# Kernel tuning notes

Hardware: AMD Instinct MI355X
Metric: run time of the kernel (lower is better)

The kernel has to match this reference:

```python
import jax, jax.numpy as jnp
import numpy as np

K = 20        # kNN neighborhood size (args.k)
EPS = 1e-5    # BatchNorm eps
SLOPE = 0.2   # LeakyReLU negative slope
B, N = 8, 2048


def lrelu(x):
    return jnp.where(x >= 0, x, SLOPE * x)


def bn_cn(x):  # BatchNorm1d over [B, C, N] (training-mode batch stats, gamma=1, beta=0)
    m = jnp.mean(x, axis=(0, 2), keepdims=True)
    v = jnp.var(x, axis=(0, 2), keepdims=True)
    return (x - m) * jax.lax.rsqrt(v + EPS)


def bn_f(x):  # BatchNorm1d over [B, F]
    m = jnp.mean(x, axis=0, keepdims=True)
    v = jnp.var(x, axis=0, keepdims=True)
    return (x - m) * jax.lax.rsqrt(v + EPS)


def conv_bn(x, w):  # 1x1 Conv1d (no bias) + BN + LeakyReLU; x [B,C,N], w [O,C]
    return lrelu(bn_cn(jnp.einsum('oc,bcn->bon', w, x)))


def knn_idx(x, k):  # x [B,C,N] -> [B,N,k] nearest neighbors, self excluded
    sq = jnp.sum(x * x, axis=1)                                   # [B,N]
    pd = 2.0 * jnp.einsum('bcn,bcm->bnm', x, x) - sq[:, :, None] - sq[:, None, :]
    return jax.lax.top_k(pd, k + 1)[1][:, :, 1:]                  # drop self (max = 0)


def self_att(x, wq, wk, wv, wc):  # SelfAttention block (n_heads=1, scale_dot)
    idx = knn_idx(x, K)                                           # [B,N,K]
    feats = jnp.swapaxes(x, 1, 2)                                 # [B,N,C]
    nb = jax.vmap(lambda f, i: f[i])(feats, idx)                  # [B,N,K,C] gather
    E = wq.shape[0]
    q = feats @ wq.T                                              # [B,N,E]
    kk = nb @ wk.T                                                # [B,N,K,E]
    v = (nb - feats[:, :, None, :]) @ wv.T                        # [B,N,K,V]
    scores = jax.nn.softmax(jnp.einsum('bne,bnke->bnk', q, kk) / np.float32(np.sqrt(E)), axis=-1)
    out = jnp.einsum('bnk,bnkv->bnv', scores, v)                  # [B,N,V]
    res = conv_bn(jnp.swapaxes(out, 1, 2), wc)                    # [B,O,N]
    return jnp.concatenate([res, x], axis=1)


def setup_inputs() -> dict:
    key = jax.random.key(0)
    ks = jax.random.split(key, 32)
    w = lambda k, o, i: jax.random.normal(k, (o, i), jnp.float32) / np.float32(np.sqrt(i))
    d = {'x': jax.random.normal(ks[0], (B, 3, N), jnp.float32)}
    dims = {1: 3, 2: 64, 3: 64, 4: 128}
    j = 1
    for s, c in dims.items():
        for nm in ('wq', 'wk', 'wv', 'wc'):
            d[f'sa{s}_{nm}'] = w(ks[j], c, c); j += 1
    d['conv1_w'] = w(ks[17], 64, 6)
    d['conv2_w'] = w(ks[18], 64, 128)
    d['conv3_w'] = w(ks[19], 128, 128)
    d['conv4_w'] = w(ks[20], 256, 256)
    d['conv5_w'] = w(ks[21], 1024, 512)
    d['lin1_w'] = w(ks[22], 512, 2048); d['lin1_b'] = jnp.zeros((512,), jnp.float32)
    d['lin2_w'] = w(ks[23], 256, 512);  d['lin2_b'] = jnp.zeros((256,), jnp.float32)
    d['lin3_w'] = w(ks[24], 40, 256);   d['lin3_b'] = jnp.zeros((40,), jnp.float32)
    return d


def reference(x, sa1_wq, sa1_wk, sa1_wv, sa1_wc, sa2_wq, sa2_wk, sa2_wv, sa2_wc,
              sa3_wq, sa3_wk, sa3_wv, sa3_wc, sa4_wq, sa4_wk, sa4_wv, sa4_wc,
              conv1_w, conv2_w, conv3_w, conv4_w, conv5_w,
              lin1_w, lin1_b, lin2_w, lin2_b, lin3_w, lin3_b):
    h = self_att(x, sa1_wq, sa1_wk, sa1_wv, sa1_wc)        # [B,6,N]
    x1 = conv_bn(h, conv1_w)                               # [B,64,N]
    h = self_att(x1, sa2_wq, sa2_wk, sa2_wv, sa2_wc)       # [B,128,N]
    x2 = conv_bn(h, conv2_w)                               # [B,64,N]
    h = self_att(x2, sa3_wq, sa3_wk, sa3_wv, sa3_wc)       # [B,128,N]
    x3 = conv_bn(h, conv3_w)                               # [B,128,N]
    h = self_att(x3, sa4_wq, sa4_wk, sa4_wv, sa4_wc)       # [B,256,N]
    x4 = conv_bn(h, conv4_w)                               # [B,256,N]
    xc = jnp.concatenate([x1, x2, x3, x4], axis=1)         # [B,512,N]
    x5 = conv_bn(xc, conv5_w)                              # [B,1024,N]
    p = jnp.concatenate([jnp.max(x5, axis=2), jnp.mean(x5, axis=2)], axis=1)  # [B,2048]
    h = lrelu(bn_f(p @ lin1_w.T + lin1_b))                 # dropout = identity (eval)
    h = lrelu(bn_f(h @ lin2_w.T + lin2_b))
    return h @ lin3_w.T + lin3_b                           # [B,40]
```

## Files before the change

kernel.cpp:

```cpp
#include <hip/hip_runtime.h>
#include <math.h>

#define BB 8
#define NN 2048
#define KNB 20

typedef __attribute__((ext_vector_type(8))) short bf16x8;
typedef __attribute__((ext_vector_type(8))) _Float16 f16x8;
typedef __attribute__((ext_vector_type(4))) float f32x4;

__device__ inline unsigned short f2bf(float f) {
  union { float f; unsigned u; } v; v.f = f;
  unsigned r = v.u + 0x7FFF + ((v.u >> 16) & 1);
  return (unsigned short)(r >> 16);
}

__device__ inline float lrelu(float v) { return v >= 0.f ? v : 0.2f * v; }

template <bool F16SPLIT, bool BF16>
__global__ __launch_bounds__(256) void xprep_kernel(
    const float* __restrict__ in, int inBS, int C,
    float* __restrict__ xT, _Float16* __restrict__ hi, _Float16* __restrict__ lo,
    unsigned short* __restrict__ bf, float* __restrict__ sq) {
  __shared__ float tile[32][33];
  __shared__ float ps[8][33];
  int b = blockIdx.z;
  const float* ip = in + (size_t)b * inBS;
  int c0 = blockIdx.x * 32;
  int r0 = blockIdx.y * 32;
  int tx = threadIdx.x & 31, ty = threadIdx.x >> 5;
  float s = 0.f;
  for (int yy = ty; yy < 32; yy += 8) {
    int r = r0 + yy;
    float v = (r < C) ? ip[(size_t)r * NN + c0 + tx] : 0.f;
    tile[yy][tx] = v;
    s += v * v;
  }
  ps[ty][tx] = s;
  __syncthreads();
  if (ty == 0) {
    float a = ps[0][tx];
#pragma unroll
    for (int u = 1; u < 8; ++u) a += ps[u][tx];
    atomicAdd(&sq[b * NN + c0 + tx], a);
  }
  for (int yy = ty; yy < 32; yy += 8) {
    int c = c0 + yy, r = r0 + tx;
    if (r < C) {
      float v = tile[tx][yy];
      size_t o = (size_t)b * NN * C + (size_t)c * C + r;
      xT[o] = v;
      if (F16SPLIT) {
        _Float16 hv = (_Float16)v;
        hi[o] = hv;
        lo[o] = (_Float16)(v - (float)hv);
      }
      if (BF16) bf[o] = f2bf(v);
    }
  }
}

__global__ __launch_bounds__(256) void prep_mw_kernel(
    const float* __restrict__ wq, const float* __restrict__ wk,
    const float* __restrict__ wv, const float* __restrict__ wc, int C,
    float* __restrict__ M, float* __restrict__ WCV,
    unsigned short* __restrict__ Mb, unsigned short* __restrict__ wcvb, int emitBF) {
  int w = blockIdx.x * 4 + (threadIdx.x >> 6);
  int lane = threadIdx.x & 63;
  int total = 2 * C * C;
  if (w >= total) return;
  float a = 0.f;
  if (w < C * C) {
    int c = w / C, cp = w - c * C;
    for (int e = lane; e < C; e += 64) a += wk[e * C + c] * wq[e * C + cp];
  } else {
    int t = w - C * C;
    int o = t / C, c = t - o * C;
    for (int e = lane; e < C; e += 64) a += wc[o * C + e] * wv[e * C + c];
  }
#pragma unroll
  for (int s = 32; s > 0; s >>= 1) a += __shfl_down(a, s);
  if (lane == 0) {
    if (w < C * C) {
      M[w] = a;
      if (emitBF) Mb[w] = f2bf(a);
    } else {
      int t = w - C * C;
      WCV[t] = a;
      if (emitBF) wcvb[t] = f2bf(a);
    }
  }
}

__global__ __launch_bounds__(256) void convert_bf16_kernel(const float* __restrict__ in,
                                                           unsigned short* __restrict__ out,
                                                           int count) {
  int i = blockIdx.x * 256 + threadIdx.x;
  if (i < count) out[i] = f2bf(in[i]);
}

__global__ __launch_bounds__(256) void transpose_kernel(const float* __restrict__ in, int inBS,
                                                        int R, int Cl, float* __restrict__ out) {
  __shared__ float tile[32][33];
  int b = blockIdx.z;
  const float* ip = in + (size_t)b * inBS;
  float* op = out + (size_t)b * R * Cl;
  int c0 = blockIdx.x * 32, r0 = blockIdx.y * 32;
  int tx = threadIdx.x & 31, ty = threadIdx.x >> 5;
  for (int yy = ty; yy < 32; yy += 8) {
    int r = r0 + yy, c = c0 + tx;
    tile[yy][tx] = (r < R && c < Cl) ? ip[(size_t)r * Cl + c] : 0.f;
  }
  __syncthreads();
  for (int yy = ty; yy < 32; yy += 8) {
    int c = c0 + yy, r = r0 + tx;
    if (c < Cl && r < R) op[(size_t)c * R + r] = tile[tx][yy];
  }
}

__global__ __launch_bounds__(256) void transpose_bf16_kernel(const float* __restrict__ in, int inBS,
                                                             int R, int Cl,
                                                             unsigned short* __restrict__ out) {
  __shared__ float tile[32][33];
  int b = blockIdx.z;
  const float* ip = in + (size_t)b * inBS;
  unsigned short* op = out + (size_t)b * R * Cl;
  int c0 = blockIdx.x * 32, r0 = blockIdx.y * 32;
  int tx = threadIdx.x & 31, ty = threadIdx.x >> 5;
  for (int yy = ty; yy < 32; yy += 8) {
    int r = r0 + yy, c = c0 + tx;
    tile[yy][tx] = (r < R && c < Cl) ? ip[(size_t)r * Cl + c] : 0.f;
  }
  __syncthreads();
  for (int yy = ty; yy < 32; yy += 8) {
    int c = c0 + yy, r = r0 + tx;
    if (c < Cl && r < R) op[(size_t)c * R + r] = f2bf(tile[tx][yy]);
  }
}

__global__ __launch_bounds__(256, 2) void mfma_gemm_lds_kernel(
    const unsigned short* __restrict__ A, const unsigned short* __restrict__ B,
    float* __restrict__ Z, int O, int K) {
  const int b = blockIdx.z;
  const int n0 = blockIdx.x * 128, o0 = blockIdx.y * 128;
  const int tid = threadIdx.x;
  const int wave = tid >> 6, lane = tid & 63;
  const int wo = wave >> 1, wn = wave & 1;
  const int l16 = lane & 15, q = lane >> 4;
  __shared__ unsigned short Al[2][4096];
  __shared__ unsigned short Bl[2][4096];
  const unsigned short* Ab = A + (size_t)o0 * K;
  const unsigned short* Bb = B + ((size_t)b * NN + n0) * K;

  const int p0 = tid, p1 = tid + 256;
  const int r0 = ((p0 >> 6) << 4) | (p0 & 15), c0 = ((p0 >> 4) & 3) * 8;
  const int r1 = ((p1 >> 6) << 4) | (p1 & 15), c1 = ((p1 >> 4) & 3) * 8;

  bf16x8 ar0, ar1, br0, br1;
  auto gload = [&](int k0) {
    ar0 = *(const bf16x8*)(Ab + (size_t)r0 * K + k0 + c0);
    ar1 = *(const bf16x8*)(Ab + (size_t)r1 * K + k0 + c1);
    br0 = *(const bf16x8*)(Bb + (size_t)r0 * K + k0 + c0);
    br1 = *(const bf16x8*)(Bb + (size_t)r1 * K + k0 + c1);
  };
  auto sstore = [&](int buf) {
    *(bf16x8*)&Al[buf][p0 * 8] = ar0;
    *(bf16x8*)&Al[buf][p1 * 8] = ar1;
    *(bf16x8*)&Bl[buf][p0 * 8] = br0;
    *(bf16x8*)&Bl[buf][p1 * 8] = br1;
  };

  f32x4 acc[4][4];
#pragma unroll
  for (int s = 0; s < 4; ++s)
#pragma unroll
    for (int t = 0; t < 4; ++t) acc[s][t] = (f32x4){0.f, 0.f, 0.f, 0.f};

  gload(0);
  sstore(0);
  int cur = 0;
  for (int k0 = 0; k0 < K; k0 += 32) {
    bool more = (k0 + 32) < K;
    if (more) gload(k0 + 32);
    __syncthreads();
    bf16x8 af[4], bfr[4];
#pragma unroll
    for (int s = 0; s < 4; ++s)
      af[s] = *(const bf16x8*)&Al[cur][((wo * 4 + s) * 64 + q * 16 + l16) * 8];
#pragma unroll
    for (int t = 0; t < 4; ++t)
      bfr[t] = *(const bf16x8*)&Bl[cur][((wn * 4 + t) * 64 + q * 16 + l16) * 8];
#pragma unroll
    for (int s = 0; s < 4; ++s)
#pragma unroll
      for (int t = 0; t < 4; ++t)
        acc[s][t] = __builtin_amdgcn_mfma_f32_16x16x32_bf16(af[s], bfr[t], acc[s][t], 0, 0, 0);
    if (more) sstore(cur ^ 1);
    cur ^= 1;
  }
#pragma unroll
  for (int s = 0; s < 4; ++s)
#pragma unroll
    for (int t = 0; t < 4; ++t) {
      float* zp = Z + ((size_t)b * O + o0 + wo * 64 + s * 16 + q * 4) * NN
                  + n0 + wn * 64 + t * 16 + l16;
#pragma unroll
      for (int r = 0; r < 4; ++r) zp[(size_t)r * NN] = acc[s][t][r];
    }
}

__global__ __launch_bounds__(256, 2) void pd_mfma_kernel(
    const _Float16* __restrict__ xhi, const _Float16* __restrict__ xlo, int C,
    const float* __restrict__ sq, float* __restrict__ P, int b_base) {
  const int bl = blockIdx.z;
  const int b = b_base + bl;
  const int n0 = blockIdx.x * 128, m0 = blockIdx.y * 128;
  const int tid = threadIdx.x;
  const int wave = tid >> 6, lane = tid & 63;
  const int wn_ = wave >> 1, wm_ = wave & 1;
  const int l16 = lane & 15, q = lane >> 4;
  __shared__ _Float16 Ah[4096], Al[4096], Bh[4096], Bl[4096];
  const _Float16* Ahg = xhi + ((size_t)b * NN + n0) * C;
  const _Float16* Alg = xlo + ((size_t)b * NN + n0) * C;
  const _Float16* Bhg = xhi + ((size_t)b * NN + m0) * C;
  const _Float16* Blg = xlo + ((size_t)b * NN + m0) * C;

  const int p0 = tid, p1 = tid + 256;
  const int r0 = ((p0 >> 6) << 4) | (p0 & 15), c0 = ((p0 >> 4) & 3) * 8;
  const int r1 = ((p1 >> 6) << 4) | (p1 & 15), c1 = ((p1 >> 4) & 3) * 8;

  f32x4 acc[4][4];
#pragma unroll
  for (int s = 0; s < 4; ++s)
#pragma unroll
    for (int t = 0; t < 4; ++t) acc[s][t] = (f32x4){0.f, 0.f, 0.f, 0.f};

  for (int k0 = 0; k0 < C; k0 += 32) {
    __syncthreads();
    *(f16x8*)&Ah[p0 * 8] = *(const f16x8*)(Ahg + (size_t)r0 * C + k0 + c0);
    *(f16x8*)&Ah[p1 * 8] = *(const f16x8*)(Ahg + (size_t)r1 * C + k0 + c1);
    *(f16x8*)&Al[p0 * 8] = *(const f16x8*)(Alg + (size_t)r0 * C + k0 + c0);
    *(f16x8*)&Al[p1 * 8] = *(const f16x8*)(Alg + (size_t)r1 * C + k0 + c1);
    *(f16x8*)&Bh[p0 * 8] = *(const f16x8*)(Bhg + (size_t)r0 * C + k0 + c0);
    *(f16x8*)&Bh[p1 * 8] = *(const f16x8*)(Bhg + (size_t)r1 * C + k0 + c1);
    *(f16x8*)&Bl[p0 * 8] = *(const f16x8*)(Blg + (size_t)r0 * C + k0 + c0);
    *(f16x8*)&Bl[p1 * 8] = *(const f16x8*)(Blg + (size_t)r1 * C + k0 + c1);
    __syncthreads();
    f16x8 ah[4], al[4], bh[4], blv[4];
#pragma unroll
    for (int s = 0; s < 4; ++s) {
      int pi = ((wn_ * 4 + s) * 64 + q * 16 + l16) * 8;
      ah[s] = *(const f16x8*)&Ah[pi];
      al[s] = *(const f16x8*)&Al[pi];
    }
#pragma unroll
    for (int t = 0; t < 4; ++t) {
      int pi = ((wm_ * 4 + t) * 64 + q * 16 + l16) * 8;
      bh[t] = *(const f16x8*)&Bh[pi];
      blv[t] = *(const f16x8*)&Bl[pi];
    }
#pragma unroll
    for (int s = 0; s < 4; ++s)
#pragma unroll
      for (int t = 0; t < 4; ++t) {
        acc[s][t] = __builtin_amdgcn_mfma_f32_16x16x32_f16(ah[s], bh[t], acc[s][t], 0, 0, 0);
        acc[s][t] = __builtin_amdgcn_mfma_f32_16x16x32_f16(ah[s], blv[t], acc[s][t], 0, 0, 0);
        acc[s][t] = __builtin_amdgcn_mfma_f32_16x16x32_f16(al[s], bh[t], acc[s][t], 0, 0, 0);
      }
  }
#pragma unroll
  for (int s = 0; s < 4; ++s)
#pragma unroll
    for (int t = 0; t < 4; ++t) {
      int col = m0 + wm_ * 64 + t * 16 + l16;
      float sqv = sq[b * NN + col];
      float* pp = P + ((size_t)bl * NN + n0 + wn_ * 64 + s * 16 + q * 4) * NN + col;
#pragma unroll
      for (int r = 0; r < 4; ++r) pp[(size_t)r * NN] = 2.f * acc[s][t][r] - sqv;
    }
}

__global__ __launch_bounds__(256, 2) void pd_gemm128_db_kernel(
    const float* __restrict__ x, int bs, int C, const float* __restrict__ sq,
    float* __restrict__ P, int b_base) {
  const int b = b_base + blockIdx.z;
  const int n0 = blockIdx.x * 128, m0 = blockIdx.y * 128;
  const int tid = threadIdx.x;
  const int tm = tid & 15, tn = tid >> 4;
  __shared__ float As[2][16][128], Bs[2][16][128];
  const float* xb = x + (size_t)b * bs;
  float acc[8][8];
#pragma unroll
  for (int i = 0; i < 8; ++i)
#pragma unroll
    for (int j = 0; j < 8; ++j) acc[i][j] = 0.f;

  float4 ara[2], arb[2];
  auto load_tile = [&](int k0) {
#pragma unroll
    for (int it = 0; it < 2; ++it) {
      int i = it * 256 + tid;
      int kc = i >> 5, c4 = i & 31;
      bool ok = (k0 + kc) < C;
      ara[it] = ok ? *(const float4*)&xb[(size_t)(k0 + kc) * NN + n0 + c4 * 4]
                   : make_float4(0.f, 0.f, 0.f, 0.f);
      arb[it] = ok ? *(const float4*)&xb[(size_t)(k0 + kc) * NN + m0 + c4 * 4]
                   : make_float4(0.f, 0.f, 0.f, 0.f);
    }
  };
  auto store_tile = [&](int buf) {
#pragma unroll
    for (int it = 0; it < 2; ++it) {
      int i = it * 256 + tid;
      int kc = i >> 5, c4 = i & 31;
      *(float4*)&As[buf][kc][c4 * 4] = ara[it];
      *(float4*)&Bs[buf][kc][c4 * 4] = arb[it];
    }
  };

  load_tile(0);
  store_tile(0);
  int cur = 0;
  for (int k0 = 0; k0 < C; k0 += 16) {
    bool more = (k0 + 16) < C;
    if (more) load_tile(k0 + 16);
    __syncthreads();
#pragma unroll
    for (int kc = 0; kc < 16; ++kc) {
      float4 a0 = *(const float4*)&As[cur][kc][tn * 4];
      float4 a1 = *(const float4*)&As[cur][kc][64 + tn * 4];
      float4 b0 = *(const float4*)&Bs[cur][kc][tm * 4];
      float4 b1 = *(const float4*)&Bs[cur][kc][64 + tm * 4];
      float ar[8] = {a0.x, a0.y, a0.z, a0.w, a1.x, a1.y, a1.z, a1.w};
      float br[8] = {b0.x, b0.y, b0.z, b0.w, b1.x, b1.y, b1.z, b1.w};
#pragma unroll
      for (int i = 0; i < 8; ++i)
#pragma unroll
        for (int j = 0; j < 8; ++j) acc[i][j] += ar[i] * br[j];
    }
    if (more) store_tile(cur ^ 1);
    cur ^= 1;
  }
  float4 sqa = *(const float4*)&sq[b * NN + m0 + tm * 4];
  float4 sqb = *(const float4*)&sq[b * NN + m0 + 64 + tm * 4];
#pragma unroll
  for (int h = 0; h < 2; ++h)
#pragma unroll
    for (int i = 0; i < 4; ++i) {
      int r = h * 4 + i;
      int nn = n0 + h * 64 + tn * 4 + i;
      float* prow = &P[((size_t)blockIdx.z * NN + nn) * NN + m0];
      float4 o0, o1;
      o0.x = 2.f * acc[r][0] - sqa.x; o0.y = 2.f * acc[r][1] - sqa.y;
      o0.z = 2.f * acc[r][2] - sqa.z; o0.w = 2.f * acc[r][3] - sqa.w;
      o1.x = 2.f * acc[r][4] - sqb.x; o1.y = 2.f * acc[r][5] - sqb.y;
      o1.z = 2.f * acc[r][6] - sqb.z; o1.w = 2.f * acc[r][7] - sqb.w;
      *(float4*)&prow[tm * 4] = o0;
      *(float4*)&prow[64 + tm * 4] = o1;
    }
}

__global__ __launch_bounds__(256) void topk_bsort_kernel(const float* __restrict__ P,
                                                         int* __restrict__ idx_out, int b_base) {
  const int wave = threadIdx.x >> 6;
  const int lane = threadIdx.x & 63;
  const int n = blockIdx.x * 4 + wave;
  const int bl = blockIdx.y;
  const int b = b_base + bl;
  const float4* rp = (const float4*)(P + ((size_t)bl * NN + n) * NN);
  unsigned key[32], mv[32];
#pragma unroll
  for (int q = 0; q < 8; ++q) {
    float4 vv = rp[q * 64 + lane];
    int mb = q * 256 + lane * 4;
    float fv[4] = {vv.x, vv.y, vv.z, vv.w};
#pragma unroll
    for (int j = 0; j < 4; ++j) {
      unsigned u = __float_as_uint(fv[j]);
      unsigned mask = (unsigned)(((int)u) >> 31) | 0x80000000u;
      key[q * 4 + j] = (mb + j == n) ? 0u : (u ^ mask);
      mv[q * 4 + j] = (unsigned)(mb + j);
    }
  }
#pragma unroll
  for (int k = 2; k <= 32; k <<= 1) {
#pragma unroll
    for (int j = k >> 1; j > 0; j >>= 1) {
#pragma unroll
      for (int i = 0; i < 32; ++i) {
        int l = i ^ j;
        if (l > i) {
          unsigned ka = key[i], kb = key[l];
          unsigned ia = mv[i], ib = mv[l];
          bool agt = ka > kb;
          unsigned kmax = agt ? ka : kb, kmin = agt ? kb : ka;
          unsigned imax = agt ? ia : ib, imin = agt ? ib : ia;
          if ((i & k) == 0) { key[i] = kmax; mv[i] = imax; key[l] = kmin; mv[l] = imin; }
          else              { key[i] = kmin; mv[i] = imin; key[l] = kmax; mv[l] = imax; }
        }
      }
    }
  }
  int* op = idx_out + (size_t)(b * NN + n) * KNB;
  for (int k = 0; k < KNB; ++k) {
    unsigned best = key[0];
#pragma unroll
    for (int s = 32; s > 0; s >>= 1) {
      unsigned o = (unsigned)__shfl_xor((int)best, s);
      best = best > o ? best : o;
    }
    bool own = (key[0] == best);
    if (own) {
      op[k] = (int)mv[0];
#pragma unroll
      for (int j = 0; j < 20; ++j) { key[j] = key[j + 1]; mv[j] = mv[j + 1]; }
    }
  }
}

__global__ __launch_bounds__(256, 2) void conv_gemm_kernel(
    const float* __restrict__ in, int inBS, int C, int O,
    const float* __restrict__ w, float* __restrict__ z) {
  const int b = blockIdx.z;
  const int n0 = blockIdx.x * 64, o0 = blockIdx.y * 64;
  const int tid = threadIdx.x;
  const int tm = tid & 15, tn = tid >> 4;
  __shared__ float Ws[16][68];
  __shared__ float Xs[16][64];
  const float* ib = in + (size_t)b * inBS;
  float acc[4][4];
#pragma unroll
  for (int i = 0; i < 4; ++i)
#pragma unroll
    for (int j = 0; j < 4; ++j) acc[i][j] = 0.f;

  for (int k0 = 0; k0 < C; k0 += 16) {
    __syncthreads();
#pragma unroll
    for (int it = 0; it < 4; ++it) {
      int i = it * 256 + tid;
      int kc = i >> 6, nl = i & 63;
      Xs[kc][nl] = ((k0 + kc) < C) ? ib[(size_t)(k0 + kc) * NN + n0 + nl] : 0.f;
      int ol = i >> 4, kc2 = i & 15;
      Ws[kc2][ol] = ((o0 + ol) < O && (k0 + kc2) < C) ? w[(size_t)(o0 + ol) * C + k0 + kc2] : 0.f;
    }
    __syncthreads();
#pragma unroll
    for (int kc = 0; kc < 16; ++kc) {
      float4 a = *(const float4*)&Ws[kc][tn * 4];
      float4 bv = *(const float4*)&Xs[kc][tm * 4];
      acc[0][0] += a.x * bv.x; acc[0][1] += a.x * bv.y; acc[0][2] += a.x * bv.z; acc[0][3] += a.x * bv.w;
      acc[1][0] += a.y * bv.x; acc[1][1] += a.y * bv.y; acc[1][2] += a.y * bv.z; acc[1][3] += a.y * bv.w;
      acc[2][0] += a.z * bv.x; acc[2][1] += a.z * bv.y; acc[2][2] += a.z * bv.z; acc[2][3] += a.z * bv.w;
      acc[3][0] += a.w * bv.x; acc[3][1] += a.w * bv.y; acc[3][2] += a.w * bv.z; acc[3][3] += a.w * bv.w;
    }
  }
#pragma unroll
  for (int i = 0; i < 4; ++i) {
    int o = o0 + tn * 4 + i;
    if (o < O) {
      float4 ov;
      ov.x = acc[i][0]; ov.y = acc[i][1]; ov.z = acc[i][2]; ov.w = acc[i][3];
      *(float4*)&z[((size_t)b * O + o) * NN + n0 + tm * 4] = ov;
    }
  }
}

__global__ __launch_bounds__(256, 2) void conv_gemm128_db_kernel(
    const float* __restrict__ in, int inBS, int C, int O,
    const float* __restrict__ w, float* __restrict__ z) {
  const int b = blockIdx.z;
  const int n0 = blockIdx.x * 128, o0 = blockIdx.y * 128;
  const int tid = threadIdx.x;
  const int tm = tid & 15, tn = tid >> 4;
  __shared__ float Xs[2][16][128];
  __shared__ float Ws[2][16][132];
  const float* ib = in + (size_t)b * inBS;
  float acc[8][8];
#pragma unroll
  for (int i = 0; i < 8; ++i)
#pragma unroll
    for (int j = 0; j < 8; ++j) acc[i][j] = 0.f;

  float4 xr[2], wr[2];
  auto load_tile = [&](int k0) {
#pragma unroll
    for (int it = 0; it < 2; ++it) {
      int i = it * 256 + tid;
      int kc = i >> 5, c4 = i & 31;
      xr[it] = ((k0 + kc) < C) ? *(const float4*)&ib[(size_t)(k0 + kc) * NN + n0 + c4 * 4]
                               : make_float4(0.f, 0.f, 0.f, 0.f);
      int ol = i >> 2, kq = i & 3;
      wr[it] = ((k0 + kq * 4) < C) ? *(const float4*)&w[(size_t)(o0 + ol) * C + k0 + kq * 4]
                                   : make_float4(0.f, 0.f, 0.f, 0.f);
    }
  };
  auto store_tile = [&](int buf) {
#pragma unroll
    for (int it = 0; it < 2; ++it) {
      int i = it * 256 + tid;
      int kc = i >> 5, c4 = i & 31;
      *(float4*)&Xs[buf][kc][c4 * 4] = xr[it];
      int ol = i >> 2, kq = i & 3;
      Ws[buf][kq * 4 + 0][ol] = wr[it].x;
      Ws[buf][kq * 4 + 1][ol] = wr[it].y;
      Ws[buf][kq * 4 + 2][ol] = wr[it].z;
      Ws[buf][kq * 4 + 3][ol] = wr[it].w;
    }
  };

  load_tile(0);
  store_tile(0);
  int cur = 0;
  for (int k0 = 0; k0 < C; k0 += 16) {
    bool more = (k0 + 16) < C;
    if (more) load_tile(k0 + 16);
    __syncthreads();
#pragma unroll
    for (int kc = 0; kc < 16; ++kc) {
      float4 a0 = *(const float4*)&Ws[cur][kc][tn * 4];
      float4 a1 = *(const float4*)&Ws[cur][kc][64 + tn * 4];
      float4 b0 = *(const float4*)&Xs[cur][kc][tm * 4];
      float4 b1 = *(const float4*)&Xs[cur][kc][64 + tm * 4];
      float ar[8] = {a0.x, a0.y, a0.z, a0.w, a1.x, a1.y, a1.z, a1.w};
      float br[8] = {b0.x, b0.y, b0.z, b0.w, b1.x, b1.y, b1.z, b1.w};
#pragma unroll
      for (int i = 0; i < 8; ++i)
#pragma unroll
        for (int j = 0; j < 8; ++j) acc[i][j] += ar[i] * br[j];
    }
    if (more) store_tile(cur ^ 1);
    cur ^= 1;
  }
#pragma unroll
  for (int h = 0; h < 2; ++h)
#pragma unroll
    for (int i = 0; i < 4; ++i) {
      int r = h * 4 + i;
      int o = o0 + h * 64 + tn * 4 + i;
      float* zrow = &z[((size_t)b * O + o) * NN + n0];
      float4 o0v, o1v;
      o0v.x = acc[r][0]; o0v.y = acc[r][1]; o0v.z = acc[r][2]; o0v.w = acc[r][3];
      o1v.x = acc[r][4]; o1v.y = acc[r][5]; o1v.z = acc[r][6]; o1v.w = acc[r][7];
      *(float4*)&zrow[tm * 4] = o0v;
      *(float4*)&zrow[64 + tm * 4] = o1v;
    }
}

template <int C, bool BF16OUT>
__global__ __launch_bounds__(64) void att_wave_kernel(
    const float* __restrict__ xT, const float* __restrict__ UT,
    const int* __restrict__ idx, float* __restrict__ AGGt,
    unsigned short* __restrict__ AGGtb) {
  const int n = blockIdx.x & (NN - 1);
  const int b = blockIdx.x >> 11;
  const int lane = threadIdx.x;
  constexpr int CP = C + 1;
  __shared__ float nb[KNB][CP];
  __shared__ float sl[KNB];
  __shared__ int nidx[KNB];
  __shared__ float ul[C];
  const float* xTb = xT + (size_t)b * NN * C;
  if (lane < KNB) nidx[lane] = idx[(size_t)(b * NN + n) * KNB + lane];
  for (int c = lane; c < C; c += 64) ul[c] = UT[((size_t)b * NN + n) * C + c];
  __syncthreads();
  for (int i = lane; i < KNB * C; i += 64) {
    int k = i / C, c = i - k * C;
    nb[k][c] = xTb[(size_t)nidx[k] * C + c];
  }
  __syncthreads();
  float sv = -INFINITY;
  if (lane < KNB) {
    float a = 0.f;
#pragma unroll
    for (int c = 0; c < C; ++c) a += nb[lane][c] * ul[c];
    sv = a / sqrtf((float)C);
  }
  float mx = sv;
#pragma unroll
  for (int s = 32; s > 0; s >>= 1) mx = fmaxf(mx, __shfl_xor(mx, s));
  float e = (lane < KNB) ? expf(sv - mx) : 0.f;
  float sum = e;
#pragma unroll
  for (int s = 32; s > 0; s >>= 1) sum += __shfl_xor(sum, s);
  if (lane < KNB) sl[lane] = e / sum;
  __syncthreads();
  const float* xTn = xTb + (size_t)n * C;
  for (int c = lane; c < C; c += 64) {
    float a = 0.f;
#pragma unroll
    for (int k = 0; k < KNB; ++k) a += sl[k] * nb[k][c];
    float r = a - xTn[c];
    if (BF16OUT)
      AGGtb[((size_t)b * NN + n) * C + c] = f2bf(r);
    else
      AGGt[((size_t)b * NN + n) * C + c] = r;
  }
}

__global__ __launch_bounds__(256) void bn_fused_kernel(const float* __restrict__ z, int O,
                                                       float* __restrict__ out, int outBS, int c0) {
  int o = blockIdx.x;
  int tid = threadIdx.x;
  __shared__ float s1[256], s2[256];
  __shared__ float smv, srv;
  float a1 = 0.f, a2 = 0.f;
  for (int i = tid; i < BB * 512; i += 256) {
    int b = i >> 9, n4 = i & 511;
    float4 v = *(const float4*)&z[((size_t)b * O + o) * NN + n4 * 4];
    a1 += v.x + v.y + v.z + v.w;
    a2 += v.x * v.x + v.y * v.y + v.z * v.z + v.w * v.w;
  }
  s1[tid] = a1; s2[tid] = a2;
  __syncthreads();
  for (int st = 128; st > 0; st >>= 1) {
    if (tid < st) { s1[tid] += s1[tid + st]; s2[tid] += s2[tid + st]; }
    __syncthreads();
  }
  if (tid == 0) {
    float m = s1[0] / (BB * NN);
    float var = s2[0] / (BB * NN) - m * m;
    smv = m; srv = rsqrtf(var + 1e-5f);
  }
  __syncthreads();
  float m = smv, r = srv;
  for (int i = tid; i < BB * 512; i += 256) {
    int b = i >> 9, n4 = i & 511;
    float4 v = *(const float4*)&z[((size_t)b * O + o) * NN + n4 * 4];
    float4 ov;
    ov.x = lrelu((v.x - m) * r); ov.y = lrelu((v.y - m) * r);
    ov.z = lrelu((v.z - m) * r); ov.w = lrelu((v.w - m) * r);
    *(float4*)&out[(size_t)b * outBS + (size_t)(c0 + o) * NN + n4 * 4] = ov;
  }
}

__global__ __launch_bounds__(256) void bn_copy_kernel(const float* __restrict__ z, int O,
                                                      const float* __restrict__ xin, int xbs,
                                                      float* __restrict__ out) {
  int o = blockIdx.x;
  int tid = threadIdx.x;
  int outBS = 2 * O * NN;
  if (o >= O) {
    int c = o - O;
    for (int i = tid; i < BB * 512; i += 256) {
      int b = i >> 9, n4 = i & 511;
      *(float4*)&out[(size_t)b * outBS + (size_t)o * NN + n4 * 4] =
          *(const float4*)&xin[(size_t)b * xbs + (size_t)c * NN + n4 * 4];
    }
    return;
  }
  __shared__ float s1[256], s2[256];
  __shared__ float smv, srv;
  float a1 = 0.f, a2 = 0.f;
  for (int i = tid; i < BB * 512; i += 256) {
    int b = i >> 9, n4 = i & 511;
    float4 v = *(const float4*)&z[((size_t)b * O + o) * NN + n4 * 4];
    a1 += v.x + v.y + v.z + v.w;
    a2 += v.x * v.x + v.y * v.y + v.z * v.z + v.w * v.w;
  }
  s1[tid] = a1; s2[tid] = a2;
  __syncthreads();
  for (int st = 128; st > 0; st >>= 1) {
    if (tid < st) { s1[tid] += s1[tid + st]; s2[tid] += s2[tid + st]; }
    __syncthreads();
  }
  if (tid == 0) {
    float m = s1[0] / (BB * NN);
    float var = s2[0] / (BB * NN) - m * m;
    smv = m; srv = rsqrtf(var + 1e-5f);
  }
  __syncthreads();
  float m = smv, r = srv;
  for (int i = tid; i < BB * 512; i += 256) {
    int b = i >> 9, n4 = i & 511;
    float4 v = *(const float4*)&z[((size_t)b * O + o) * NN + n4 * 4];
    float4 ov;
    ov.x = lrelu((v.x - m) * r); ov.y = lrelu((v.y - m) * r);
    ov.z = lrelu((v.z - m) * r); ov.w = lrelu((v.w - m) * r);
    *(float4*)&out[(size_t)b * outBS + (size_t)o * NN + n4 * 4] = ov;
  }
}

__global__ __launch_bounds__(256) void bn_pool_kernel(const float* __restrict__ z,
                                                      float* __restrict__ p) {
  int o = blockIdx.x;
  int tid = threadIdx.x;
  __shared__ float s1[256], s2[256];
  __shared__ float smv, srv;
  float a1 = 0.f, a2 = 0.f;
  for (int i = tid; i < BB * 512; i += 256) {
    int b = i >> 9, n4 = i & 511;
    float4 v = *(const float4*)&z[((size_t)b * 1024 + o) * NN + n4 * 4];
    a1 += v.x + v.y + v.z + v.w;
    a2 += v.x * v.x + v.y * v.y + v.z * v.z + v.w * v.w;
  }
  s1[tid] = a1; s2[tid] = a2;
  __syncthreads();
  for (int st = 128; st > 0; st >>= 1) {
    if (tid < st) { s1[tid] += s1[tid + st]; s2[tid] += s2[tid + st]; }
    __syncthreads();
  }
  if (tid == 0) {
    float m = s1[0] / (BB * NN);
    float var = s2[0] / (BB * NN) - m * m;
    smv = m; srv = rsqrtf(var + 1e-5f);
  }
  __syncthreads();
  float m = smv, r = srv;
  int b = tid >> 5, l = tid & 31;
  const float* zp = z + ((size_t)b * 1024 + o) * NN;
  float mx = -INFINITY, sm = 0.f;
  for (int j = l; j < 512; j += 32) {
    float4 v = *(const float4*)&zp[j * 4];
    float vx = lrelu((v.x - m) * r), vy = lrelu((v.y - m) * r);
    float vz = lrelu((v.z - m) * r), vw = lrelu((v.w - m) * r);
    mx = fmaxf(mx, fmaxf(fmaxf(vx, vy), fmaxf(vz, vw)));
    sm += vx + vy + vz + vw;
  }
#pragma unroll
  for (int s = 16; s > 0; s >>= 1) {
    mx = fmaxf(mx, __shfl_xor(mx, s));
    sm += __shfl_xor(sm, s);
  }
  if (l == 0) {
    p[b * 2048 + o] = mx;
    p[b * 2048 + 1024 + o] = sm * (1.f / NN);
  }
}

__global__ __launch_bounds__(64) void linear_kernel(const float* __restrict__ in, int IN, int OUT,
                                                    const float* __restrict__ w,
                                                    const float* __restrict__ bias,
                                                    float* __restrict__ out) {
  int o = blockIdx.x;
  int b = o / OUT, f = o % OUT;
  const float* ip = in + (size_t)b * IN;
  const float* wp = w + (size_t)f * IN;
  float a = 0.f;
  for (int i = threadIdx.x; i < IN; i += 64) a += ip[i] * wp[i];
#pragma unroll
  for (int s = 32; s > 0; s >>= 1) a += __shfl_down(a, s);
  if (threadIdx.x == 0) out[o] = a + bias[f];
}

__global__ __launch_bounds__(256) void bnf_kernel(float* __restrict__ t, int F) {
  int f = blockIdx.x * blockDim.x + threadIdx.x;
  if (f >= F) return;
  float s = 0.f, s2 = 0.f;
  for (int b = 0; b < BB; ++b) { float v = t[b * F + f]; s += v; s2 += v * v; }
  float m = s * (1.f / BB);
  float var = s2 * (1.f / BB) - m * m;
  float r = rsqrtf(var + 1e-5f);
  for (int b = 0; b < BB; ++b) {
    float v = (t[b * F + f] - m) * r;
    t[b * F + f] = v >= 0.f ? v : 0.2f * v;
  }
}


struct SAW { const float *wq, *wk, *wv, *wc; };

static inline void run_conv(const float* in, int inBS, int C, int O, const float* w,
                            float* z, hipStream_t st) {
  if (O % 128 == 0)
    conv_gemm128_db_kernel<<<dim3(NN / 128, O / 128, BB), 256, 0, st>>>(in, inBS, C, O, w, z);
  else
    conv_gemm_kernel<<<dim3(NN / 64, (O + 63) / 64, BB), 256, 0, st>>>(in, inBS, C, O, w, z);
}

template <int C, bool MFMA>
static inline void run_sa(const float* xin, int xbs, SAW w,
                          float* xT, float* U, float* UT, float* AGGt,
                          float* AGG, float* z, float* h, float* sq, int* idx,
                          float* M, float* WCV, unsigned short* Mb, unsigned short* wcvb,
                          unsigned short* xTb, unsigned short* AGGtb,
                          _Float16* xhi, _Float16* xlo,
                          float* D, int nbatch, hipStream_t st) {
  constexpr bool PDM = (C % 32 == 0);
  hipMemsetAsync(sq, 0, (size_t)BB * NN * 4, st);
  xprep_kernel<PDM, MFMA><<<dim3(NN / 32, (C + 31) / 32, BB), 256, 0, st>>>(
      xin, xbs, C, xT, xhi, xlo, xTb, sq);
  prep_mw_kernel<<<(2 * C * C + 3) / 4, 256, 0, st>>>(w.wq, w.wk, w.wv, w.wc, C,
                                                      M, WCV, Mb, wcvb, MFMA ? 1 : 0);
  for (int bb = 0; bb < BB; bb += nbatch) {
    int nbc = (BB - bb) < nbatch ? (BB - bb) : nbatch;
    if (PDM)
      pd_mfma_kernel<<<dim3(16, 16, nbc), 256, 0, st>>>(xhi, xlo, C, sq, D, bb);
    else
      pd_gemm128_db_kernel<<<dim3(NN / 128, NN / 128, nbc), 256, 0, st>>>(xin, xbs, C, sq, D, bb);
    topk_bsort_kernel<<<dim3(NN / 4, nbc), 256, 0, st>>>(D, idx, bb);
  }
  if (MFMA)
    mfma_gemm_lds_kernel<<<dim3(NN / 128, C / 128, BB), 256, 0, st>>>(Mb, xTb, U, C, C);
  else
    run_conv(xin, xbs, C, C, M, U, st);
  transpose_kernel<<<dim3(NN / 32, (C + 31) / 32, BB), 256, 0, st>>>(U, C * NN, C, NN, UT);
  if (MFMA) {
    att_wave_kernel<C, true><<<BB * NN, 64, 0, st>>>(xT, UT, idx, AGGt, AGGtb);
    mfma_gemm_lds_kernel<<<dim3(NN / 128, C / 128, BB), 256, 0, st>>>(wcvb, AGGtb, z, C, C);
  } else {
    att_wave_kernel<C, false><<<BB * NN, 64, 0, st>>>(xT, UT, idx, AGGt, AGGtb);
    transpose_kernel<<<dim3((C + 31) / 32, NN / 32, BB), 256, 0, st>>>(AGGt, NN * C, NN, C, AGG);
    run_conv(AGG, C * NN, C, C, WCV, z, st);
  }
  bn_copy_kernel<<<2 * C, 256, 0, st>>>(z, C, xin, xbs, h);
}

static inline void run_conv_bn(const float* in, int inBS, int Cin, int O, const float* w,
                               float* z, float* out, int outBS, int c0, hipStream_t st) {
  run_conv(in, inBS, Cin, O, w, z, st);
  bn_fused_kernel<<<O, 256, 0, st>>>(z, O, out, outBS, c0);
}

extern "C" void kernel_launch(void* const* d_in, const int* in_sizes, int n_in,
                              void* d_out, int out_size, void* d_ws, size_t ws_size,
                              hipStream_t stream) {
  const float* x = (const float*)d_in[0];
  SAW sa1{(const float*)d_in[1], (const float*)d_in[2], (const float*)d_in[3], (const float*)d_in[4]};
  SAW sa2{(const float*)d_in[5], (const float*)d_in[6], (const float*)d_in[7], (const float*)d_in[8]};
  SAW sa3{(const float*)d_in[9], (const float*)d_in[10], (const float*)d_in[11], (const float*)d_in[12]};
  SAW sa4{(const float*)d_in[13], (const float*)d_in[14], (const float*)d_in[15], (const float*)d_in[16]};
  const float* conv1_w = (const float*)d_in[17];
  const float* conv2_w = (const float*)d_in[18];
  const float* conv3_w = (const float*)d_in[19];
  const float* conv4_w = (const float*)d_in[20];
  const float* conv5_w = (const float*)d_in[21];
  const float* lin1_w = (const float*)d_in[22];
  const float* lin1_b = (const float*)d_in[23];
  const float* lin2_w = (const float*)d_in[24];
  const float* lin2_b = (const float*)d_in[25];
  const float* lin3_w = (const float*)d_in[26];
  const float* lin3_b = (const float*)d_in[27];

  char* ws = (char*)d_ws;
  size_t off = 0;
  auto take = [&](size_t bytes) -> void* {
    void* p = ws + off;
    off += (bytes + 255) & ~(size_t)255;
    return p;
  };
  float* sq   = (float*)take((size_t)BB * NN * 4);
  int*   idx  = (int*)take((size_t)BB * NN * KNB * 4);
  float* M    = (float*)take((size_t)128 * 128 * 4);
  float* WCV  = (float*)take((size_t)128 * 128 * 4);
  unsigned short* Mb   = (unsigned short*)take((size_t)128 * 128 * 2);
  unsigned short* wcvb = (unsigned short*)take((size_t)128 * 128 * 2);
  unsigned short* w4b  = (unsigned short*)take((size_t)256 * 256 * 2);
  unsigned short* w5b  = (unsigned short*)take((size_t)1024 * 512 * 2);
  float* U    = (float*)take((size_t)BB * 128 * NN * 4);
  float* AGG  = (float*)take((size_t)BB * 128 * NN * 4);
  float* h    = (float*)take((size_t)BB * 256 * NN * 4);
  float* z    = (float*)take((size_t)BB * 1024 * NN * 4);
  float* xc   = (float*)take((size_t)BB * 512 * NN * 4);
  float* p    = (float*)take((size_t)BB * 2048 * 4);
  float* t1   = (float*)take((size_t)BB * 512 * 4);
  float* t2   = (float*)take((size_t)BB * 256 * 4);
  (void)n_in; (void)in_sizes; (void)out_size;

  float* xT = AGG;
  float* UT = h;
  float* AGGt = z;
  unsigned short* xTb   = (unsigned short*)((char*)h + (size_t)BB * 128 * NN * 4);
  unsigned short* AGGtb = (unsigned short*)((char*)z + (size_t)16 * 1024 * 1024);
  unsigned short* hTb   = (unsigned short*)U;
  unsigned short* xcTb  = (unsigned short*)U;
  _Float16* xhi = (_Float16*)h;
  _Float16* xlo = (_Float16*)((char*)h + (size_t)BB * NN * 128 * 2);

  size_t dfull = (size_t)BB * NN * NN * 4;
  bool fullD = (ws_size > off + dfull + 4096);
  float* D = fullD ? (float*)take(dfull) : z;
  int nbatch = fullD ? BB : 4;

  run_sa<3, false>(x, 3 * NN, sa1, xT, U, UT, AGGt, AGG, z, h, sq, idx,
                   M, WCV, Mb, wcvb, xTb, AGGtb, xhi, xlo, D, nbatch, stream);
  run_conv_bn(h, 6 * NN, 6, 64, conv1_w, z, xc, 512 * NN, 0, stream);
  run_sa<64, false>(xc + 0 * NN, 512 * NN, sa2, xT, U, UT, AGGt, AGG, z, h, sq, idx,
                    M, WCV, Mb, wcvb, xTb, AGGtb, xhi, xlo, D, nbatch, stream);
  run_conv_bn(h, 128 * NN, 128, 64, conv2_w, z, xc, 512 * NN, 64, stream);
  run_sa<64, false>(xc + 64 * NN, 512 * NN, sa3, xT, U, UT, AGGt, AGG, z, h, sq, idx,
                    M, WCV, Mb, wcvb, xTb, AGGtb, xhi, xlo, D, nbatch, stream);
  run_conv_bn(h, 128 * NN, 128, 128, conv3_w, z, xc, 512 * NN, 128, stream);
  run_sa<128, true>(xc + 128 * NN, 512 * NN, sa4, xT, U, UT, AGGt, AGG, z, h, sq, idx,
                    M, WCV, Mb, wcvb, xTb, AGGtb, xhi, xlo, D, nbatch, stream);
  transpose_bf16_kernel<<<dim3(NN / 32, 8, BB), 256, 0, stream>>>(h, 256 * NN, 256, NN, hTb);
  convert_bf16_kernel<<<(256 * 256 + 255) / 256, 256, 0, stream>>>(conv4_w, w4b, 256 * 256);
  mfma_gemm_lds_kernel<<<dim3(NN / 128, 2, BB), 256, 0, stream>>>(w4b, hTb, z, 256, 256);
  bn_fused_kernel<<<256, 256, 0, stream>>>(z, 256, xc, 512 * NN, 256);
  transpose_bf16_kernel<<<dim3(NN / 32, 16, BB), 256, 0, stream>>>(xc, 512 * NN, 512, NN, xcTb);
  convert_bf16_kernel<<<(1024 * 512 + 255) / 256, 256, 0, stream>>>(conv5_w, w5b, 1024 * 512);
  mfma_gemm_lds_kernel<<<dim3(NN / 128, 8, BB), 256, 0, stream>>>(w5b, xcTb, z, 1024, 512);
  bn_pool_kernel<<<1024, 256, 0, stream>>>(z, p);
  linear_kernel<<<BB * 512, 64, 0, stream>>>(p, 2048, 512, lin1_w, lin1_b, t1);
  bnf_kernel<<<2, 256, 0, stream>>>(t1, 512);
  linear_kernel<<<BB * 256, 64, 0, stream>>>(t1, 512, 256, lin2_w, lin2_b, t2);
  bnf_kernel<<<1, 256, 0, stream>>>(t2, 256);
  linear_kernel<<<BB * 40, 64, 0, stream>>>(t2, 256, 40, lin3_w, lin3_b, (float*)d_out);
}
```

Measured before the change: 968.2 us.

## Fuse C=3 kNN into a direct top-k kernel and pack indices into sort keys

```diff
diff --git a/kernel.cpp b/kernel.cpp
--- a/kernel.cpp
+++ b/kernel.cpp
@@ -60,6 +60,19 @@
   }
 }
 
+__global__ __launch_bounds__(256) void xprep3_kernel(const float* __restrict__ in,
+                                                     float* __restrict__ xT,
+                                                     float* __restrict__ xs4) {
+  int b = blockIdx.z;
+  int n = blockIdx.x * 256 + threadIdx.x;
+  const float* ip = in + (size_t)b * 3 * NN;
+  float x0 = ip[n], x1 = ip[NN + n], x2 = ip[2 * NN + n];
+  float s = x0 * x0 + x1 * x1 + x2 * x2;
+  size_t o = (size_t)b * NN + n;
+  xT[o * 3 + 0] = x0; xT[o * 3 + 1] = x1; xT[o * 3 + 2] = x2;
+  *(float4*)&xs4[o * 4] = make_float4(x0, x1, x2, s);
+}
+
 __global__ __launch_bounds__(256) void prep_mw_kernel(
     const float* __restrict__ wq, const float* __restrict__ wk,
     const float* __restrict__ wv, const float* __restrict__ wc, int C,
@@ -280,86 +293,6 @@
     }
 }
 
-__global__ __launch_bounds__(256, 2) void pd_gemm128_db_kernel(
-    const float* __restrict__ x, int bs, int C, const float* __restrict__ sq,
-    float* __restrict__ P, int b_base) {
-  const int b = b_base + blockIdx.z;
-  const int n0 = blockIdx.x * 128, m0 = blockIdx.y * 128;
-  const int tid = threadIdx.x;
-  const int tm = tid & 15, tn = tid >> 4;
-  __shared__ float As[2][16][128], Bs[2][16][128];
-  const float* xb = x + (size_t)b * bs;
-  float acc[8][8];
-#pragma unroll
-  for (int i = 0; i < 8; ++i)
-#pragma unroll
-    for (int j = 0; j < 8; ++j) acc[i][j] = 0.f;
-
-  float4 ara[2], arb[2];
-  auto load_tile = [&](int k0) {
-#pragma unroll
-    for (int it = 0; it < 2; ++it) {
-      int i = it * 256 + tid;
-      int kc = i >> 5, c4 = i & 31;
-      bool ok = (k0 + kc) < C;
-      ara[it] = ok ? *(const float4*)&xb[(size_t)(k0 + kc) * NN + n0 + c4 * 4]
-                   : make_float4(0.f, 0.f, 0.f, 0.f);
-      arb[it] = ok ? *(const float4*)&xb[(size_t)(k0 + kc) * NN + m0 + c4 * 4]
-                   : make_float4(0.f, 0.f, 0.f, 0.f);
-    }
-  };
-  auto store_tile = [&](int buf) {
-#pragma unroll
-    for (int it = 0; it < 2; ++it) {
-      int i = it * 256 + tid;
-      int kc = i >> 5, c4 = i & 31;
-      *(float4*)&As[buf][kc][c4 * 4] = ara[it];
-      *(float4*)&Bs[buf][kc][c4 * 4] = arb[it];
-    }
-  };
-
-  load_tile(0);
-  store_tile(0);
-  int cur = 0;
-  for (int k0 = 0; k0 < C; k0 += 16) {
-    bool more = (k0 + 16) < C;
-    if (more) load_tile(k0 + 16);
-    __syncthreads();
-#pragma unroll
-    for (int kc = 0; kc < 16; ++kc) {
-      float4 a0 = *(const float4*)&As[cur][kc][tn * 4];
-      float4 a1 = *(const float4*)&As[cur][kc][64 + tn * 4];
-      float4 b0 = *(const float4*)&Bs[cur][kc][tm * 4];
-      float4 b1 = *(const float4*)&Bs[cur][kc][64 + tm * 4];
-      float ar[8] = {a0.x, a0.y, a0.z, a0.w, a1.x, a1.y, a1.z, a1.w};
-      float br[8] = {b0.x, b0.y, b0.z, b0.w, b1.x, b1.y, b1.z, b1.w};
-#pragma unroll
-      for (int i = 0; i < 8; ++i)
-#pragma unroll
-        for (int j = 0; j < 8; ++j) acc[i][j] += ar[i] * br[j];
-    }
-    if (more) store_tile(cur ^ 1);
-    cur ^= 1;
-  }
-  float4 sqa = *(const float4*)&sq[b * NN + m0 + tm * 4];
-  float4 sqb = *(const float4*)&sq[b * NN + m0 + 64 + tm * 4];
-#pragma unroll
-  for (int h = 0; h < 2; ++h)
-#pragma unroll
-    for (int i = 0; i < 4; ++i) {
-      int r = h * 4 + i;
-      int nn = n0 + h * 64 + tn * 4 + i;
-      float* prow = &P[((size_t)blockIdx.z * NN + nn) * NN + m0];
-      float4 o0, o1;
-      o0.x = 2.f * acc[r][0] - sqa.x; o0.y = 2.f * acc[r][1] - sqa.y;
-      o0.z = 2.f * acc[r][2] - sqa.z; o0.w = 2.f * acc[r][3] - sqa.w;
-      o1.x = 2.f * acc[r][4] - sqb.x; o1.y = 2.f * acc[r][5] - sqb.y;
-      o1.z = 2.f * acc[r][6] - sqb.z; o1.w = 2.f * acc[r][7] - sqb.w;
-      *(float4*)&prow[tm * 4] = o0;
-      *(float4*)&prow[64 + tm * 4] = o1;
-    }
-}
-
 __global__ __launch_bounds__(256) void topk_bsort_kernel(const float* __restrict__ P,
                                                          int* __restrict__ idx_out, int b_base) {
   const int wave = threadIdx.x >> 6;
@@ -368,7 +301,7 @@
   const int bl = blockIdx.y;
   const int b = b_base + bl;
   const float4* rp = (const float4*)(P + ((size_t)bl * NN + n) * NN);
-  unsigned key[32], mv[32];
+  unsigned key[32];
 #pragma unroll
   for (int q = 0; q < 8; ++q) {
     float4 vv = rp[q * 64 + lane];
@@ -378,8 +311,8 @@
     for (int j = 0; j < 4; ++j) {
       unsigned u = __float_as_uint(fv[j]);
       unsigned mask = (unsigned)(((int)u) >> 31) | 0x80000000u;
-      key[q * 4 + j] = (mb + j == n) ? 0u : (u ^ mask);
-      mv[q * 4 + j] = (unsigned)(mb + j);
+      unsigned sl = (unsigned)(q * 4 + j);
+      key[q * 4 + j] = (mb + j == n) ? sl : (((u ^ mask) & 0xFFFFFFE0u) | sl);
     }
   }
 #pragma unroll
@@ -391,12 +324,10 @@
         int l = i ^ j;
         if (l > i) {
           unsigned ka = key[i], kb = key[l];
-          unsigned ia = mv[i], ib = mv[l];
-          bool agt = ka > kb;
-          unsigned kmax = agt ? ka : kb, kmin = agt ? kb : ka;
-          unsigned imax = agt ? ia : ib, imin = agt ? ib : ia;
-          if ((i & k) == 0) { key[i] = kmax; mv[i] = imax; key[l] = kmin; mv[l] = imin; }
-          else              { key[i] = kmin; mv[i] = imin; key[l] = kmax; mv[l] = imax; }
+          unsigned mx = ka > kb ? ka : kb;
+          unsigned mn = ka > kb ? kb : ka;
+          if ((i & k) == 0) { key[i] = mx; key[l] = mn; }
+          else              { key[i] = mn; key[l] = mx; }
         }
       }
     }
@@ -409,11 +340,66 @@
       unsigned o = (unsigned)__shfl_xor((int)best, s);
       best = best > o ? best : o;
     }
-    bool own = (key[0] == best);
-    if (own) {
-      op[k] = (int)mv[0];
-#pragma unroll
-      for (int j = 0; j < 20; ++j) { key[j] = key[j + 1]; mv[j] = mv[j + 1]; }
+    unsigned long long bal = __ballot(key[0] == best);
+    if (lane == (int)__ffsll(bal) - 1) {
+      unsigned sl = key[0] & 31u;
+      op[k] = (int)((sl >> 2) * 256u + (unsigned)lane * 4u + (sl & 3u));
+#pragma unroll
+      for (int j = 0; j < 20; ++j) key[j] = key[j + 1];
+    }
+  }
+}
+
+__global__ __launch_bounds__(256) void topk_c3_kernel(const float* __restrict__ xs4,
+                                                      int* __restrict__ idx_out) {
+  const int wave = threadIdx.x >> 6;
+  const int lane = threadIdx.x & 63;
+  const int n = blockIdx.x * 4 + wave;
+  const int b = blockIdx.y;
+  const float4* xp = (const float4*)(xs4 + (size_t)b * NN * 4);
+  float4 me = xp[n];
+  float tx = 2.f * me.x, ty = 2.f * me.y, tz = 2.f * me.z;
+  unsigned key[32];
+#pragma unroll
+  for (int s = 0; s < 32; ++s) {
+    int m = s * 64 + lane;
+    float4 c = xp[m];
+    float pd = tx * c.x + ty * c.y + tz * c.z - c.w;
+    unsigned u = __float_as_uint(pd);
+    unsigned mask = (unsigned)(((int)u) >> 31) | 0x80000000u;
+    key[s] = (m == n) ? (unsigned)s : ((((u ^ mask) & 0xFFFFFFE0u)) | (unsigned)s);
+  }
+#pragma unroll
+  for (int k = 2; k <= 32; k <<= 1) {
+#pragma unroll
+    for (int j = k >> 1; j > 0; j >>= 1) {
+#pragma unroll
+      for (int i = 0; i < 32; ++i) {
+        int l = i ^ j;
+        if (l > i) {
+          unsigned ka = key[i], kb = key[l];
+          unsigned mx = ka > kb ? ka : kb;
+          unsigned mn = ka > kb ? kb : ka;
+          if ((i & k) == 0) { key[i] = mx; key[l] = mn; }
+          else              { key[i] = mn; key[l] = mx; }
+        }
+      }
+    }
+  }
+  int* op = idx_out + (size_t)(b * NN + n) * KNB;
+  for (int k = 0; k < KNB; ++k) {
+    unsigned best = key[0];
+#pragma unroll
+    for (int s = 32; s > 0; s >>= 1) {
+      unsigned o = (unsigned)__shfl_xor((int)best, s);
+      best = best > o ? best : o;
+    }
+    unsigned long long bal = __ballot(key[0] == best);
+    if (lane == (int)__ffsll(bal) - 1) {
+      unsigned sl = key[0] & 31u;
+      op[k] = (int)(sl * 64u + (unsigned)lane);
+#pragma unroll
+      for (int j = 0; j < 20; ++j) key[j] = key[j + 1];
     }
   }
 }
@@ -776,34 +762,47 @@
                           unsigned short* xTb, unsigned short* AGGtb,
                           _Float16* xhi, _Float16* xlo,
                           float* D, int nbatch, hipStream_t st) {
-  constexpr bool PDM = (C % 32 == 0);
-  hipMemsetAsync(sq, 0, (size_t)BB * NN * 4, st);
-  xprep_kernel<PDM, MFMA><<<dim3(NN / 32, (C + 31) / 32, BB), 256, 0, st>>>(
+  static_assert(C % 32 == 0, "run_sa requires C % 32 == 0");
+  xprep_kernel<true, MFMA><<<dim3(NN / 32, C / 32, BB), 256, 0, st>>>(
       xin, xbs, C, xT, xhi, xlo, xTb, sq);
   prep_mw_kernel<<<(2 * C * C + 3) / 4, 256, 0, st>>>(w.wq, w.wk, w.wv, w.wc, C,
                                                       M, WCV, Mb, wcvb, MFMA ? 1 : 0);
   for (int bb = 0; bb < BB; bb += nbatch) {
     int nbc = (BB - bb) < nbatch ? (BB - bb) : nbatch;
-    if (PDM)
-      pd_mfma_kernel<<<dim3(16, 16, nbc), 256, 0, st>>>(xhi, xlo, C, sq, D, bb);
-    else
-      pd_gemm128_db_kernel<<<dim3(NN / 128, NN / 128, nbc), 256, 0, st>>>(xin, xbs, C, sq, D, bb);
+    pd_mfma_kernel<<<dim3(16, 16, nbc), 256, 0, st>>>(xhi, xlo, C, sq, D, bb);
     topk_bsort_kernel<<<dim3(NN / 4, nbc), 256, 0, st>>>(D, idx, bb);
   }
   if (MFMA)
     mfma_gemm_lds_kernel<<<dim3(NN / 128, C / 128, BB), 256, 0, st>>>(Mb, xTb, U, C, C);
   else
     run_conv(xin, xbs, C, C, M, U, st);
-  transpose_kernel<<<dim3(NN / 32, (C + 31) / 32, BB), 256, 0, st>>>(U, C * NN, C, NN, UT);
+  transpose_kernel<<<dim3(NN / 32, C / 32, BB), 256, 0, st>>>(U, C * NN, C, NN, UT);
   if (MFMA) {
     att_wave_kernel<C, true><<<BB * NN, 64, 0, st>>>(xT, UT, idx, AGGt, AGGtb);
     mfma_gemm_lds_kernel<<<dim3(NN / 128, C / 128, BB), 256, 0, st>>>(wcvb, AGGtb, z, C, C);
   } else {
     att_wave_kernel<C, false><<<BB * NN, 64, 0, st>>>(xT, UT, idx, AGGt, AGGtb);
-    transpose_kernel<<<dim3((C + 31) / 32, NN / 32, BB), 256, 0, st>>>(AGGt, NN * C, NN, C, AGG);
+    transpose_kernel<<<dim3(C / 32, NN / 32, BB), 256, 0, st>>>(AGGt, NN * C, NN, C, AGG);
     run_conv(AGG, C * NN, C, C, WCV, z, st);
   }
   bn_copy_kernel<<<2 * C, 256, 0, st>>>(z, C, xin, xbs, h);
+}
+
+static inline void run_sa3(const float* xin, SAW w,
+                           float* xT, float* U, float* UT, float* AGGt, float* AGG,
+                           float* z, float* h, float* xs4, int* idx,
+                           float* M, float* WCV, unsigned short* Mb, unsigned short* wcvb,
+                           hipStream_t st) {
+  xprep3_kernel<<<dim3(NN / 256, 1, BB), 256, 0, st>>>(xin, xT, xs4);
+  prep_mw_kernel<<<(2 * 3 * 3 + 3) / 4, 256, 0, st>>>(w.wq, w.wk, w.wv, w.wc, 3,
+                                                      M, WCV, Mb, wcvb, 0);
+  topk_c3_kernel<<<dim3(NN / 4, BB), 256, 0, st>>>(xs4, idx);
+  conv_gemm_kernel<<<dim3(NN / 64, 1, BB), 256, 0, st>>>(xin, 3 * NN, 3, 3, M, U);
+  transpose_kernel<<<dim3(NN / 32, 1, BB), 256, 0, st>>>(U, 3 * NN, 3, NN, UT);
+  att_wave_kernel<3, false><<<BB * NN, 64, 0, st>>>(xT, UT, idx, AGGt, nullptr);
+  transpose_kernel<<<dim3(1, NN / 32, BB), 256, 0, st>>>(AGGt, NN * 3, NN, 3, AGG);
+  conv_gemm_kernel<<<dim3(NN / 64, 1, BB), 256, 0, st>>>(AGG, 3 * NN, 3, 3, WCV, z);
+  bn_copy_kernel<<<6, 256, 0, st>>>(z, 3, xin, 3 * NN, h);
 }
 
 static inline void run_conv_bn(const float* in, int inBS, int Cin, int O, const float* w,
@@ -839,7 +838,8 @@
     off += (bytes + 255) & ~(size_t)255;
     return p;
   };
-  float* sq   = (float*)take((size_t)BB * NN * 4);
+  float* sqR  = (float*)take((size_t)3 * BB * NN * 4);
+  float* xs4  = (float*)take((size_t)BB * NN * 4 * 4);
   int*   idx  = (int*)take((size_t)BB * NN * KNB * 4);
   float* M    = (float*)take((size_t)128 * 128 * 4);
   float* WCV  = (float*)take((size_t)128 * 128 * 4);
@@ -872,17 +872,21 @@
   float* D = fullD ? (float*)take(dfull) : z;
   int nbatch = fullD ? BB : 4;
 
-  run_sa<3, false>(x, 3 * NN, sa1, xT, U, UT, AGGt, AGG, z, h, sq, idx,
-                   M, WCV, Mb, wcvb, xTb, AGGtb, xhi, xlo, D, nbatch, stream);
+  hipMemsetAsync(sqR, 0, (size_t)3 * BB * NN * 4, stream);
+
+  run_sa3(x, sa1, xT, U, UT, AGGt, AGG, z, h, xs4, idx, M, WCV, Mb, wcvb, stream);
   run_conv_bn(h, 6 * NN, 6, 64, conv1_w, z, xc, 512 * NN, 0, stream);
-  run_sa<64, false>(xc + 0 * NN, 512 * NN, sa2, xT, U, UT, AGGt, AGG, z, h, sq, idx,
-                    M, WCV, Mb, wcvb, xTb, AGGtb, xhi, xlo, D, nbatch, stream);
+  run_sa<64, false>(xc + 0 * NN, 512 * NN, sa2, xT, U, UT, AGGt, AGG, z, h,
+                    sqR + 0 * BB * NN, idx, M, WCV, Mb, wcvb, xTb, AGGtb, xhi, xlo,
+                    D, nbatch, stream);
   run_conv_bn(h, 128 * NN, 128, 64, conv2_w, z, xc, 512 * NN, 64, stream);
-  run_sa<64, false>(xc + 64 * NN, 512 * NN, sa3, xT, U, UT, AGGt, AGG, z, h, sq, idx,
-                    M, WCV, Mb, wcvb, xTb, AGGtb, xhi, xlo, D, nbatch, stream);
+  run_sa<64, false>(xc + 64 * NN, 512 * NN, sa3, xT, U, UT, AGGt, AGG, z, h,
+                    sqR + 1 * BB * NN, idx, M, WCV, Mb, wcvb, xTb, AGGtb, xhi, xlo,
+                    D, nbatch, stream);
   run_conv_bn(h, 128 * NN, 128, 128, conv3_w, z, xc, 512 * NN, 128, stream);
-  run_sa<128, true>(xc + 128 * NN, 512 * NN, sa4, xT, U, UT, AGGt, AGG, z, h, sq, idx,
-                    M, WCV, Mb, wcvb, xTb, AGGtb, xhi, xlo, D, nbatch, stream);
+  run_sa<128, true>(xc + 128 * NN, 512 * NN, sa4, xT, U, UT, AGGt, AGG, z, h,
+                    sqR + 2 * BB * NN, idx, M, WCV, Mb, wcvb, xTb, AGGtb, xhi, xlo,
+                    D, nbatch, stream);
   transpose_bf16_kernel<<<dim3(NN / 32, 8, BB), 256, 0, stream>>>(h, 256 * NN, 256, NN, hTb);
   convert_bf16_kernel<<<(256 * 256 + 255) / 256, 256, 0, stream>>>(conv4_w, w4b, 256 * 256);
   mfma_gemm_lds_kernel<<<dim3(NN / 128, 2, BB), 256, 0, stream>>>(w4b, hTb, z, 256, 256);
```

Result: faster. 868.7 us (-10.3%).
